# Kernel optimization log

Measured on AMD Instinct MI355X. Metric: run time of the kernel, lower is better.

The kernel has to match this reference:

```python
import jax, jax.numpy as jnp
import numpy as np

B, S, H, A, F = 16, 512, 768, 12, 3072
DH = H // A  # 64
EPS = 1e-5

def layernorm(x, w, b):
    mu = jnp.mean(x, axis=-1, keepdims=True)
    var = jnp.mean(jnp.square(x - mu), axis=-1, keepdims=True)
    return (x - mu) * jax.lax.rsqrt(var + EPS) * w + b

def setup_inputs() -> dict:
    key = jax.random.key(0)
    ks = jax.random.split(key, 12)
    std = 0.02
    inp = {
        "X": jax.random.normal(ks[0], (B, S, H), jnp.float32),
        "mask": jax.random.randint(ks[1], (B, S), 0, 2, jnp.int32),
        "WQ": jax.random.normal(ks[2], (H, H), jnp.float32) * std,
        "bQ": jnp.zeros((H,), jnp.float32),
        "WK": jax.random.normal(ks[3], (H, H), jnp.float32) * std,
        "bK": jnp.zeros((H,), jnp.float32),
        "WV": jax.random.normal(ks[4], (H, H), jnp.float32) * std,
        "bV": jnp.zeros((H,), jnp.float32),
        "WO": jax.random.normal(ks[5], (H, H), jnp.float32) * std,
        "bO": jnp.zeros((H,), jnp.float32),
        "ln1_w": jnp.ones((H,), jnp.float32),
        "ln1_b": jnp.zeros((H,), jnp.float32),
        "W1": jax.random.normal(ks[6], (H, F), jnp.float32) * std,
        "b1": jnp.zeros((F,), jnp.float32),
        "W2": jax.random.normal(ks[7], (F, H), jnp.float32) * std,
        "b2": jnp.zeros((H,), jnp.float32),
        "ln2_w": jnp.ones((H,), jnp.float32),
        "ln2_b": jnp.zeros((H,), jnp.float32),
    }
    return inp

def reference(X, mask, WQ, bQ, WK, bK, WV, bV, WO, bO, ln1_w, ln1_b, W1, b1, W2, b2, ln2_w, ln2_b):
    # --- multi-head self-attention (pretrained-weights branch, faithful reshapes) ---
    Q = (X @ WQ + bQ).reshape(B, A, S, DH)
    K = (X @ WK + bK).reshape(B, A, S, DH)
    V = (X @ WV + bV).reshape(B, A, S, DH)
    scores = jnp.einsum('bhqd,bhkd->bhqk', Q, K) / jnp.sqrt(jnp.float32(DH))
    scores = jnp.where(mask[:, None, None, :] == 0, -jnp.inf, scores)
    attn = jax.nn.softmax(scores, axis=-1)
    Z = jnp.einsum('bhqk,bhkd->bhqd', attn, V).reshape(B, S, H)
    attn_out = Z @ WO + bO
    # residual + LN (dropout is identity in eval)
    X = layernorm(attn_out + X, ln1_w, ln1_b)
    # --- FFN with exact GELU ---
    ffn = jax.nn.gelu(X @ W1 + b1, approximate=False) @ W2 + b2
    X = layernorm(ffn + X, ln2_w, ln2_b)
    return X
```

## Files before the change

### kernel.cpp

```cpp
#include <hip/hip_runtime.h>
#include <hip/hip_bf16.h>


using bf16_t = __hip_bfloat16;
typedef __bf16 bf16x8 __attribute__((ext_vector_type(8)));
typedef float f32x4 __attribute__((ext_vector_type(4)));
typedef float f32x16 __attribute__((ext_vector_type(16)));

__device__ __forceinline__ float b2f(bf16_t v) { return __bfloat162float(v); }
__device__ __forceinline__ bf16_t f2b(float v) { return __float2bfloat16(v); }
__device__ __forceinline__ ushort f2bu(float v) { bf16_t b = f2b(v); return *(ushort*)&b; }

__device__ __forceinline__ void glds16(const ushort* g, ushort* l) {
    __builtin_amdgcn_global_load_lds(
        (const __attribute__((address_space(1))) unsigned int*)g,
        (__attribute__((address_space(3))) unsigned int*)l, 16, 0, 0);
}

__device__ __forceinline__ float gelu_f(float x) {
    float x2 = x * x;
    float y2 = 1.5957691216057308f * x * fmaf(0.044715f, x2, 1.0f);
    float e = __expf(y2);
    float t = 1.f - 2.f / (e + 1.f);
    return 0.5f * x * (1.f + t);
}

__device__ __forceinline__ void tr_tile(const float* __restrict__ in,
                                        bf16_t* __restrict__ out,
                                        int R, int C, int tx, int ty,
                                        float (*t)[65], int tid)
{
    int r0 = ty * 64, c0 = tx * 64;
    int tr = tid >> 6, tc = tid & 63;
#pragma unroll 4
    for (int i = 0; i < 16; ++i) {
        int r = i * 4 + tr;
        t[r][tc] = in[(size_t)(r0 + r) * C + c0 + tc];
    }
    __syncthreads();
#pragma unroll 4
    for (int i = 0; i < 16; ++i) {
        int r = i * 4 + tr;
        out[(size_t)(c0 + r) * R + r0 + tc] = f2b(t[tc][r]);
    }
}

__global__ __launch_bounds__(256) void prep_kernel(
    const float* __restrict__ WQ, const float* __restrict__ WK,
    const float* __restrict__ WV, const float* __restrict__ WO,
    const float* __restrict__ W1, const float* __restrict__ W2,
    const float* __restrict__ bQ, const float* __restrict__ bK,
    const float* __restrict__ bV, const float* __restrict__ X,
    bf16_t* __restrict__ Wqkv, bf16_t* __restrict__ WOt,
    bf16_t* __restrict__ W1t, bf16_t* __restrict__ W2t,
    float* __restrict__ bcat, bf16_t* __restrict__ Xb)
{
    __shared__ float t[64][65];
    const int blk = blockIdx.x, tid = threadIdx.x;
    if (blk < 576) {
        int m = blk / 144, tt = blk % 144;
        const float* in = (m == 0) ? WQ : (m == 1) ? WK : (m == 2) ? WV : WO;
        bf16_t* out = (m == 0) ? Wqkv : (m == 1) ? Wqkv + 589824
                    : (m == 2) ? Wqkv + 1179648 : WOt;
        tr_tile(in, out, 768, 768, tt % 12, tt / 12, t, tid);
    } else if (blk < 1152) {
        int tt = blk - 576;
        tr_tile(W1, W1t, 768, 3072, tt % 48, tt / 48, t, tid);
    } else if (blk < 1728) {
        int tt = blk - 1152;
        tr_tile(W2, W2t, 3072, 768, tt % 12, tt / 12, t, tid);
    } else if (blk == 1728) {
        for (int i = tid; i < 2304; i += 256)
            bcat[i] = (i < 768) ? bQ[i] : (i < 1536) ? bK[i - 768] : bV[i - 1536];
    } else {
        size_t i = ((size_t)(blk - 1729) * 256 + tid) * 8;
        float4 a = *(const float4*)(X + i);
        float4 b = *(const float4*)(X + i + 4);
#pragma unroll
        for (int j = 0; j < 4; ++j) {
            Xb[i + j]     = f2b(((const float*)&a)[j]);
            Xb[i + 4 + j] = f2b(((const float*)&b)[j]);
        }
    }
}

template <int EPI, int NTILE>
__global__ __launch_bounds__(256) void gemm128(
    const bf16_t* __restrict__ A, const bf16_t* __restrict__ Bt,
    const float* __restrict__ bias, const void* __restrict__ res,
    void* __restrict__ Cv, int K, int lda, int ldb, int ldc)
{
    __shared__ ushort lA[128 * 64];
    __shared__ ushort lB[NTILE * 64];
    constexpr int NI = NTILE / 64;
    const int tid = threadIdx.x;
    const int l = tid & 63, w = tid >> 6;
    const int l31 = l & 31, khalf = l >> 5;
    const int m0 = blockIdx.x * 128, n0 = blockIdx.y * NTILE;

    const int srow = tid >> 3;
    const int sg = (((tid & 7) ^ (srow & 7)) << 3);
    const ushort* gA = (const ushort*)A + (size_t)(m0 + srow) * lda + sg;
    const ushort* gB = (const ushort*)Bt + (size_t)(n0 + srow) * ldb + sg;
    ushort* dA = lA + tid * 8;
    ushort* dB = lB + tid * 8;

    f32x16 acc[2][NI] = {};
    const int arow = (w & 1) * 64;
    const int brow = (w >> 1) * (NTILE / 2);

    for (int k0 = 0; k0 < K; k0 += 64) {
        __syncthreads();
        glds16(gA + k0,                      dA);
        glds16(gA + k0 + (size_t)32 * lda,   dA + 2048);
        glds16(gA + k0 + (size_t)64 * lda,   dA + 4096);
        glds16(gA + k0 + (size_t)96 * lda,   dA + 6144);
        glds16(gB + k0,                      dB);
        glds16(gB + k0 + (size_t)32 * ldb,   dB + 2048);
        if constexpr (NTILE == 128) {
            glds16(gB + k0 + (size_t)64 * ldb, dB + 4096);
            glds16(gB + k0 + (size_t)96 * ldb, dB + 6144);
        }
        __syncthreads();
#pragma unroll
        for (int kk = 0; kk < 4; ++kk) {
            const int pc = (((kk * 2 + khalf) ^ (l31 & 7)) << 3);
            bf16x8 bfr[NI];
#pragma unroll
            for (int ni = 0; ni < NI; ++ni)
                bfr[ni] = *(const bf16x8*)&lB[(brow + ni * 32 + l31) * 64 + pc];
#pragma unroll
            for (int mi = 0; mi < 2; ++mi) {
                bf16x8 afr = *(const bf16x8*)&lA[(arow + mi * 32 + l31) * 64 + pc];
#pragma unroll
                for (int ni = 0; ni < NI; ++ni)
                    acc[mi][ni] = __builtin_amdgcn_mfma_f32_32x32x16_bf16(bfr[ni], afr, acc[mi][ni], 0, 0, 0);
            }
        }
    }

#pragma unroll
    for (int mi = 0; mi < 2; ++mi) {
        int m = m0 + arow + mi * 32 + l31;
#pragma unroll
        for (int ni = 0; ni < NI; ++ni) {
#pragma unroll
            for (int g = 0; g < 4; ++g) {
                int nb = n0 + brow + ni * 32 + 8 * g + 4 * khalf;
                float4 bv4 = *(const float4*)&bias[nb];
                float v[4];
#pragma unroll
                for (int r = 0; r < 4; ++r) v[r] = acc[mi][ni][g * 4 + r] + ((const float*)&bv4)[r];
                if constexpr (EPI == 1) {
#pragma unroll
                    for (int r = 0; r < 4; ++r) v[r] = gelu_f(v[r]);
                } else if constexpr (EPI == 2) {
                    float4 r4 = *(const float4*)&((const float*)res)[(size_t)m * ldc + nb];
#pragma unroll
                    for (int r = 0; r < 4; ++r) v[r] += ((const float*)&r4)[r];
                } else if constexpr (EPI == 5) {
                    ushort4 rb = *(const ushort4*)&((const ushort*)res)[(size_t)m * ldc + nb];
#pragma unroll
                    for (int r = 0; r < 4; ++r) v[r] += b2f(*(const bf16_t*)&((const ushort*)&rb)[r]);
                }
                if constexpr (EPI == 5) {
                    *(float4*)&((float*)Cv)[(size_t)m * ldc + nb] = make_float4(v[0], v[1], v[2], v[3]);
                } else {
                    ushort4 st;
                    st.x = f2bu(v[0]); st.y = f2bu(v[1]); st.z = f2bu(v[2]); st.w = f2bu(v[3]);
                    if constexpr (EPI == 6) {
                        int seg = n0 / 768;
                        int nloc = (n0 % 768) + brow + ni * 32 + 8 * g + 4 * khalf;
                        if (seg < 2) {
                            bf16_t* Cseg = (bf16_t*)Cv + (size_t)seg * 6291456;
                            *(ushort4*)&((ushort*)Cseg)[(size_t)m * 768 + nloc] = st;
                        } else {
                            ushort* vt = (ushort*)res;
                            int fb = (m & 511) * 768 + nloc;
                            int h = (m >> 9) * 12 + (fb >> 15);
                            int d = fb & 63;
                            int s = (fb >> 6) & 511;
                            ushort* vh = vt + (size_t)h * 32768 + s;
                            vh[(size_t)(d + 0) * 512] = st.x;
                            vh[(size_t)(d + 1) * 512] = st.y;
                            vh[(size_t)(d + 2) * 512] = st.z;
                            vh[(size_t)(d + 3) * 512] = st.w;
                        }
                    } else {
                        *(ushort4*)&((ushort*)Cv)[(size_t)m * ldc + nb] = st;
                    }
                }
            }
        }
    }
}

__global__ __launch_bounds__(256) void flash_kernel(
    const bf16_t* __restrict__ Q, const bf16_t* __restrict__ Kx,
    const bf16_t* __restrict__ Vt, const int* __restrict__ mask,
    bf16_t* __restrict__ Z)
{
    __shared__ ushort lK[64 * 64];
    __shared__ ushort lV[64 * 64];
    __shared__ ushort lP[128 * 72];

    const int h = blockIdx.y;
    const int q0 = blockIdx.x * 128;
    const ushort* Qh = (const ushort*)Q + (size_t)h * 32768;
    const ushort* Kh = (const ushort*)Kx + (size_t)h * 32768;
    const ushort* Vh = (const ushort*)Vt + (size_t)h * 32768;
    const int* mk = mask + (h / 12) * 512;
    ushort* Zh = (ushort*)Z + (size_t)h * 32768;

    const int tid = threadIdx.x;
    const int l = tid & 63, w = tid >> 6;
    const int l16 = l & 15, quad = l >> 4;

    bf16x8 qfr[2][2];
#pragma unroll
    for (int mi = 0; mi < 2; ++mi)
#pragma unroll
        for (int kk = 0; kk < 2; ++kk)
            qfr[mi][kk] = *(const bf16x8*)(Qh + (size_t)(q0 + w * 32 + mi * 16 + l16) * 64 + kk * 32 + quad * 8);

    const int c8p = tid & 7;
    const int kr0 = tid >> 3;
    float m_i[2] = {-1e30f, -1e30f}, l_i[2] = {0.f, 0.f};
    f32x4 o4[2][4] = {};

    for (int kt = 0; kt < 8; ++kt) {
#pragma unroll
        for (int p = 0; p < 2; ++p) {
            int row = kr0 + p * 32;
            int c8l = c8p ^ (row & 7);
            glds16(Kh + (size_t)(kt * 64 + row) * 64 + c8l * 8, lK + (p * 256 + tid) * 8);
            glds16(Vh + (size_t)row * 512 + kt * 64 + c8l * 8, lV + (p * 256 + tid) * 8);
        }
        __syncthreads();

        f32x4 s4[2][4] = {};
#pragma unroll
        for (int kk = 0; kk < 2; ++kk) {
#pragma unroll
            for (int nt = 0; nt < 4; ++nt) {
                bf16x8 kfr = *(const bf16x8*)&lK[(nt * 16 + l16) * 64 + (((kk * 4 + quad) ^ (l16 & 7)) << 3)];
#pragma unroll
                for (int mi = 0; mi < 2; ++mi)
                    s4[mi][nt] = __builtin_amdgcn_mfma_f32_16x16x32_bf16(kfr, qfr[mi][kk], s4[mi][nt], 0, 0, 0);
            }
        }

        int4 m4[4];
#pragma unroll
        for (int nt = 0; nt < 4; ++nt) m4[nt] = *(const int4*)&mk[kt * 64 + nt * 16 + quad * 4];

#pragma unroll
        for (int mi = 0; mi < 2; ++mi) {
            float pv[4][4];
            float rm = -1e30f;
#pragma unroll
            for (int nt = 0; nt < 4; ++nt)
#pragma unroll
                for (int r = 0; r < 4; ++r) {
                    float v = (((const int*)&m4[nt])[r] == 0) ? -1e30f : s4[mi][nt][r] * 0.125f;
                    pv[nt][r] = v;
                    rm = fmaxf(rm, v);
                }
            rm = fmaxf(rm, __shfl_xor(rm, 16));
            rm = fmaxf(rm, __shfl_xor(rm, 32));
            float mn = fmaxf(m_i[mi], rm);
            float al = __expf(m_i[mi] - mn);
            float rs = 0.f;
#pragma unroll
            for (int nt = 0; nt < 4; ++nt)
#pragma unroll
                for (int r = 0; r < 4; ++r) {
                    float e = __expf(pv[nt][r] - mn);
                    pv[nt][r] = e;
                    rs += e;
                }
            rs += __shfl_xor(rs, 16);
            rs += __shfl_xor(rs, 32);
            l_i[mi] = l_i[mi] * al + rs;
            m_i[mi] = mn;
#pragma unroll
            for (int dt = 0; dt < 4; ++dt)
#pragma unroll
                for (int r = 0; r < 4; ++r) o4[mi][dt][r] *= al;

#pragma unroll
            for (int nt = 0; nt < 4; ++nt) {
                ushort4 st;
                st.x = f2bu(pv[nt][0]); st.y = f2bu(pv[nt][1]);
                st.z = f2bu(pv[nt][2]); st.w = f2bu(pv[nt][3]);
                *(ushort4*)&lP[(w * 32 + mi * 16 + l16) * 72 + nt * 16 + quad * 4] = st;
            }
        }
        __syncthreads();

#pragma unroll
        for (int kk = 0; kk < 2; ++kk) {
#pragma unroll
            for (int dt = 0; dt < 4; ++dt) {
                bf16x8 bvfr = *(const bf16x8*)&lV[(dt * 16 + l16) * 64 + (((kk * 4 + quad) ^ (l16 & 7)) << 3)];
#pragma unroll
                for (int mi = 0; mi < 2; ++mi) {
                    bf16x8 pafr = *(const bf16x8*)&lP[(w * 32 + mi * 16 + l16) * 72 + kk * 32 + quad * 8];
                    o4[mi][dt] = __builtin_amdgcn_mfma_f32_16x16x32_bf16(bvfr, pafr, o4[mi][dt], 0, 0, 0);
                }
            }
        }
        __syncthreads();
    }

#pragma unroll
    for (int mi = 0; mi < 2; ++mi) {
        float inv = 1.f / l_i[mi];
#pragma unroll
        for (int dt = 0; dt < 4; ++dt) {
            ushort4 st;
            st.x = f2bu(o4[mi][dt][0] * inv); st.y = f2bu(o4[mi][dt][1] * inv);
            st.z = f2bu(o4[mi][dt][2] * inv); st.w = f2bu(o4[mi][dt][3] * inv);
            *(ushort4*)&Zh[(size_t)(q0 + w * 32 + mi * 16 + l16) * 64 + dt * 16 + quad * 4] = st;
        }
    }
}

__device__ __forceinline__ float to_f(float v)  { return v; }
__device__ __forceinline__ float to_f(bf16_t v) { return b2f(v); }
__device__ __forceinline__ void from_f(float& d, float v)  { d = v; }
__device__ __forceinline__ void from_f(bf16_t& d, float v) { d = f2b(v); }

template <typename TI, typename TO>
__global__ __launch_bounds__(256) void layernorm_kernel(
    const TI* __restrict__ X, const float* __restrict__ w,
    const float* __restrict__ b, TO* __restrict__ out)
{
    const TI* x = X + (size_t)blockIdx.x * 768;
    TO* o = out + (size_t)blockIdx.x * 768;
    int t = threadIdx.x;
    float v[3];
    float s = 0.f, sq = 0.f;
#pragma unroll
    for (int i = 0; i < 3; ++i) {
        v[i] = to_f(x[t + i * 256]);
        s += v[i]; sq += v[i] * v[i];
    }
#pragma unroll
    for (int off = 32; off; off >>= 1) { s += __shfl_xor(s, off); sq += __shfl_xor(sq, off); }
    __shared__ float s1[4], s2[4];
    int wave = t >> 6, lane = t & 63;
    if (lane == 0) { s1[wave] = s; s2[wave] = sq; }
    __syncthreads();
    s  = s1[0] + s1[1] + s1[2] + s1[3];
    sq = s2[0] + s2[1] + s2[2] + s2[3];
    float mu  = s * (1.f / 768.f);
    float var = sq * (1.f / 768.f) - mu * mu;
    float rs  = rsqrtf(var + 1e-5f);
#pragma unroll
    for (int i = 0; i < 3; ++i)
        from_f(o[t + i * 256], (v[i] - mu) * rs * w[t + i * 256] + b[t + i * 256]);
}

extern "C" void kernel_launch(void* const* d_in, const int* in_sizes, int n_in,
                              void* d_out, int out_size, void* d_ws, size_t ws_size,
                              hipStream_t stream)
{
    const float* X    = (const float*)d_in[0];
    const int*   mask = (const int*)  d_in[1];
    const float* WQ   = (const float*)d_in[2];
    const float* bQ   = (const float*)d_in[3];
    const float* WK   = (const float*)d_in[4];
    const float* bK   = (const float*)d_in[5];
    const float* WV   = (const float*)d_in[6];
    const float* bV   = (const float*)d_in[7];
    const float* WO   = (const float*)d_in[8];
    const float* bO   = (const float*)d_in[9];
    const float* ln1w = (const float*)d_in[10];
    const float* ln1b = (const float*)d_in[11];
    const float* W1   = (const float*)d_in[12];
    const float* b1   = (const float*)d_in[13];
    const float* W2   = (const float*)d_in[14];
    const float* b2   = (const float*)d_in[15];
    const float* ln2w = (const float*)d_in[16];
    const float* ln2b = (const float*)d_in[17];
    float* out = (float*)d_out;

    bf16_t* ws   = (bf16_t*)d_ws;
    bf16_t* Wqkv = ws;
    bf16_t* WOt  = Wqkv + 1769472;
    bf16_t* W1t  = WOt + 589824;
    bf16_t* W2t  = W1t + 2359296;
    float*  bcat = (float*)(W2t + 2359296);
    bf16_t* Qb   = W2t + 2359296 + 4608;
    bf16_t* Kb   = Qb + 6291456;
    bf16_t* Vb   = Kb + 6291456;
    bf16_t* Xb   = Vb + 6291456;
    bf16_t* Vt   = Xb + 6291456;
    bf16_t* Zb = Qb;
    bf16_t* Y1 = Xb;
    bf16_t* X1 = Qb;
    bf16_t* Hb = Kb;

    prep_kernel<<<4801, 256, 0, stream>>>(WQ, WK, WV, WO, W1, W2, bQ, bK, bV, X,
                                          Wqkv, WOt, W1t, W2t, bcat, Xb);

    gemm128<6, 128><<<dim3(64, 18), 256, 0, stream>>>(Xb, Wqkv, bcat, Vt, Qb,
                                                      768, 768, 768, 768);

    flash_kernel<<<dim3(4, 192), 256, 0, stream>>>(Qb, Kb, Vt, mask, Zb);

    gemm128<2, 64><<<dim3(64, 12), 256, 0, stream>>>(Zb, WOt, bO, X, Y1,
                                                     768, 768, 768, 768);
    layernorm_kernel<bf16_t, bf16_t><<<8192, 256, 0, stream>>>(Y1, ln1w, ln1b, X1);

    gemm128<1, 128><<<dim3(64, 24), 256, 0, stream>>>(X1, W1t, b1, nullptr, Hb,
                                                      768, 768, 768, 3072);
    gemm128<5, 64><<<dim3(64, 12), 256, 0, stream>>>(Hb, W2t, b2, X1, out,
                                                     3072, 3072, 3072, 768);
    layernorm_kernel<float, float><<<8192, 256, 0, stream>>>(out, ln2w, ln2b, out);
}
```

Baseline: 370.9 us.

## Add 256x256 double-buffered MFMA GEMM for QKV and FFN1 projections

Introduces a new 512-thread GEMM kernel that computes 256x256 output tiles. It double-buffers 64-wide K slices in 128KB of dynamic LDS, issuing the global-to-LDS loads for the next slice while MFMAs run on the current one, and raises wave priority around the MFMA block. The QKV projection (keeping the fused bias and V-transpose epilogue) and the FFN1 GELU GEMM now use this kernel instead of the 128-tile kernel. The aim is more operand reuse per LDS byte and loads hidden behind compute. In exchange, the large LDS footprint allows only one block per CU, and the much smaller grids (288 and 384 blocks) risk uneven tail waves across the CUs.

```diff
diff --git a/kernel.cpp b/kernel.cpp
--- a/kernel.cpp
+++ b/kernel.cpp
@@ -80,6 +80,125 @@
         for (int j = 0; j < 4; ++j) {
             Xb[i + j]     = f2b(((const float*)&a)[j]);
             Xb[i + 4 + j] = f2b(((const float*)&b)[j]);
+        }
+    }
+}
+
+template <int EPI>
+__global__ __launch_bounds__(512, 2) void gemm256(
+    const bf16_t* __restrict__ A, const bf16_t* __restrict__ Bt,
+    const float* __restrict__ bias, const void* __restrict__ res,
+    void* __restrict__ Cv, int K, int lda, int ldb, int ldc)
+{
+    extern __shared__ ushort lds[];
+    const int tid = threadIdx.x;
+    const int l31 = tid & 31, khalf = (tid >> 5) & 1;
+    const int w = tid >> 6;
+    const int wr = w >> 2, wc = w & 3;
+    const int m0 = blockIdx.x * 256, n0 = blockIdx.y * 256;
+
+    const int srow = tid >> 3;
+    const int sg = (((tid & 7) ^ (srow & 7)) << 3);
+    const ushort* gA = (const ushort*)A + (size_t)(m0 + srow) * lda + sg;
+    const ushort* gB = (const ushort*)Bt + (size_t)(n0 + srow) * ldb + sg;
+    const int dOff = tid * 8;
+
+    f32x16 acc[4][2] = {};
+    const int arow = wr * 128, brow = wc * 64;
+    const int nk = K >> 6;
+
+#pragma unroll
+    for (int p = 0; p < 4; ++p) {
+        glds16(gA + (size_t)(p * 64) * lda, lds + p * 4096 + dOff);
+        glds16(gB + (size_t)(p * 64) * ldb, lds + 16384 + p * 4096 + dOff);
+    }
+    asm volatile("s_waitcnt vmcnt(0)" ::: "memory");
+    __builtin_amdgcn_s_barrier();
+
+    for (int kt = 0; kt < nk; ++kt) {
+        const int bo = (kt & 1) << 15;
+        const ushort* sA = lds + bo;
+        const ushort* sB = lds + bo + 16384;
+        ushort* nA = lds + (bo ^ 32768);
+        ushort* nB = lds + (bo ^ 32768) + 16384;
+        const bool hasNext = (kt + 1) < nk;
+        const size_t kn = (size_t)(kt + 1) << 6;
+#pragma unroll
+        for (int kk = 0; kk < 4; ++kk) {
+            const int pc = (((kk * 2 + khalf) ^ (l31 & 7)) << 3);
+            bf16x8 afr[4], bfr[2];
+#pragma unroll
+            for (int mi = 0; mi < 4; ++mi)
+                afr[mi] = *(const bf16x8*)&sA[(arow + mi * 32 + l31) * 64 + pc];
+#pragma unroll
+            for (int ni = 0; ni < 2; ++ni)
+                bfr[ni] = *(const bf16x8*)&sB[(brow + ni * 32 + l31) * 64 + pc];
+            if (kk == 0 && hasNext) {
+#pragma unroll
+                for (int p = 0; p < 4; ++p)
+                    glds16(gA + kn + (size_t)(p * 64) * lda, nA + p * 4096 + dOff);
+            }
+            if (kk == 1 && hasNext) {
+#pragma unroll
+                for (int p = 0; p < 4; ++p)
+                    glds16(gB + kn + (size_t)(p * 64) * ldb, nB + p * 4096 + dOff);
+            }
+            __builtin_amdgcn_s_barrier();
+            asm volatile("s_waitcnt lgkmcnt(0)" ::: "memory");
+            __builtin_amdgcn_sched_barrier(0);
+            __builtin_amdgcn_s_setprio(1);
+#pragma unroll
+            for (int mi = 0; mi < 4; ++mi)
+#pragma unroll
+                for (int ni = 0; ni < 2; ++ni)
+                    acc[mi][ni] = __builtin_amdgcn_mfma_f32_32x32x16_bf16(bfr[ni], afr[mi], acc[mi][ni], 0, 0, 0);
+            __builtin_amdgcn_s_setprio(0);
+            if (kk == 3 && hasNext)
+                asm volatile("s_waitcnt vmcnt(0)" ::: "memory");
+            __builtin_amdgcn_s_barrier();
+        }
+    }
+
+#pragma unroll
+    for (int mi = 0; mi < 4; ++mi) {
+        int m = m0 + arow + mi * 32 + l31;
+#pragma unroll
+        for (int ni = 0; ni < 2; ++ni) {
+#pragma unroll
+            for (int g = 0; g < 4; ++g) {
+                int nb = n0 + brow + ni * 32 + 8 * g + 4 * khalf;
+                float4 bv4 = *(const float4*)&bias[nb];
+                float v[4];
+#pragma unroll
+                for (int r = 0; r < 4; ++r) v[r] = acc[mi][ni][g * 4 + r] + ((const float*)&bv4)[r];
+                if constexpr (EPI == 1) {
+#pragma unroll
+                    for (int r = 0; r < 4; ++r) v[r] = gelu_f(v[r]);
+                }
+                ushort4 st;
+                st.x = f2bu(v[0]); st.y = f2bu(v[1]); st.z = f2bu(v[2]); st.w = f2bu(v[3]);
+                if constexpr (EPI == 6) {
+                    int seg = n0 / 768;
+                    int nloc = (n0 % 768) + brow + ni * 32 + 8 * g + 4 * khalf;
+                    if (seg < 2) {
+                        bf16_t* Cseg = (bf16_t*)Cv + (size_t)seg * 6291456;
+                        *(ushort4*)&((ushort*)Cseg)[(size_t)m * 768 + nloc] = st;
+                    } else {
+                        ushort* vt = (ushort*)res;
+                        int fb = (m & 511) * 768 + nloc;
+                        int h = (m >> 9) * 12 + (fb >> 15);
+                        int d = fb & 63;
+                        int s = (fb >> 6) & 511;
+                        ushort* vh = vt + (size_t)h * 32768 + s;
+                        vh[(size_t)(d + 0) * 512] = st.x;
+                        vh[(size_t)(d + 1) * 512] = st.y;
+                        vh[(size_t)(d + 2) * 512] = st.z;
+                        vh[(size_t)(d + 3) * 512] = st.w;
+                    }
+                } else {
+                    *(ushort4*)&((ushort*)Cv)[(size_t)m * ldc + nb] = st;
+                }
+            }
         }
     }
 }
@@ -402,11 +521,16 @@
     bf16_t* X1 = Qb;
     bf16_t* Hb = Kb;
 
+    (void)hipFuncSetAttribute(reinterpret_cast<const void*>(&gemm256<6>),
+                              hipFuncAttributeMaxDynamicSharedMemorySize, 131072);
+    (void)hipFuncSetAttribute(reinterpret_cast<const void*>(&gemm256<1>),
+                              hipFuncAttributeMaxDynamicSharedMemorySize, 131072);
+
     prep_kernel<<<4801, 256, 0, stream>>>(WQ, WK, WV, WO, W1, W2, bQ, bK, bV, X,
                                           Wqkv, WOt, W1t, W2t, bcat, Xb);
 
-    gemm128<6, 128><<<dim3(64, 18), 256, 0, stream>>>(Xb, Wqkv, bcat, Vt, Qb,
-                                                      768, 768, 768, 768);
+    gemm256<6><<<dim3(32, 9), 512, 131072, stream>>>(Xb, Wqkv, bcat, Vt, Qb,
+                                                     768, 768, 768, 768);
 
     flash_kernel<<<dim3(4, 192), 256, 0, stream>>>(Qb, Kb, Vt, mask, Zb);
 
@@ -414,7 +538,7 @@
                                                      768, 768, 768, 768);
     layernorm_kernel<bf16_t, bf16_t><<<8192, 256, 0, stream>>>(Y1, ln1w, ln1b, X1);
 
-    gemm128<1, 128><<<dim3(64, 24), 256, 0, stream>>>(X1, W1t, b1, nullptr, Hb,
+    gemm256<1><<<dim3(32, 12), 512, 131072, stream>>>(X1, W1t, b1, nullptr, Hb,
                                                       768, 768, 768, 3072);
     gemm128<5, 64><<<dim3(64, 12), 256, 0, stream>>>(Hb, W2t, b2, X1, out,
                                                      3072, 3072, 3072, 768);
```

Result: slower. 402.3 us (+8.5%).
